# Optimization experiments

Measured on AMD Instinct MI355X. Metric: run time of the kernel, lower is better.

Reference implementation:

```python
import jax, jax.numpy as jnp
import numpy as np

SELF_DIM = 64
OBST_DIM = 32
NUM_LANDMARKS = 8
HID = 128
IN_DIM = SELF_DIM + OBST_DIM  # 96


def setup_inputs() -> dict:
    key = jax.random.key(0)
    ks = jax.random.split(key, 16)
    B = 1024
    obs = jax.random.normal(ks[0], (B, 1, SELF_DIM + 40 + NUM_LANDMARKS * OBST_DIM), dtype=jnp.float32)

    def w(k, shape, fan_in):
        return (jax.random.normal(k, shape, dtype=jnp.float32) / np.sqrt(fan_in)).astype(jnp.float32)

    return {
        "obs": obs,
        "all_neighbor_obs_size": 40,
        "batch_size": B,
        # Hypernet2: Linear(96->128), tanh, Linear(128->96*128), tanh
        "hw1": w(ks[1], (IN_DIM, HID), IN_DIM), "hb1": jnp.zeros((HID,), jnp.float32),
        "hw2": w(ks[2], (HID, IN_DIM * HID), HID), "hb2": jnp.zeros((IN_DIM * HID,), jnp.float32),
        # neighbor_value_mlp: two Linear(128->128) with tanh
        "vw1": w(ks[3], (HID, HID), HID), "vb1": jnp.zeros((HID,), jnp.float32),
        "vw2": w(ks[4], (HID, HID), HID), "vb2": jnp.zeros((HID,), jnp.float32),
        # attention_mlp: Linear(256->128) tanh, Linear(128->128) tanh, Linear(128->1)
        "aw1": w(ks[5], (2 * HID, HID), 2 * HID), "ab1": jnp.zeros((HID,), jnp.float32),
        "aw2": w(ks[6], (HID, HID), HID), "ab2": jnp.zeros((HID,), jnp.float32),
        "aw3": w(ks[7], (HID, 1), HID), "ab3": jnp.zeros((1,), jnp.float32),
    }


def reference(obs, all_neighbor_obs_size, batch_size,
              hw1, hb1, hw2, hb2, vw1, vb1, vw2, vb2,
              aw1, ab1, aw2, ab2, aw3, ab3):
    B = batch_size
    A = obs.shape[1]  # agents per row (1)
    L = NUM_LANDMARKS

    # slice obstacle block and flatten to per-obstacle rows  [B*A*L, OBST_DIM]
    obs_obstacles = obs[:, :, SELF_DIM + all_neighbor_obs_size:].reshape(-1, OBST_DIM)
    # repeat self-obs along dim 1 (torch .repeat(1, L, 1)) -> [B*A*L, SELF_DIM]
    self_rep = jnp.tile(obs[:, :, :SELF_DIM], (1, L, 1)).reshape(-1, SELF_DIM)
    mlp_input = jnp.concatenate([self_rep, obs_obstacles], axis=1)  # [N, 96]
    N = mlp_input.shape[0]

    # Hypernet2 -> per-instance weight [N, 96, HID]
    h = jnp.tanh(mlp_input @ hw1 + hb1)
    w_flat = jnp.tanh(h @ hw2 + hb2)
    obstacle_w = w_flat.reshape(N, IN_DIM, HID)

    # per-instance matvec + tanh  [N, HID]
    emb = jnp.tanh(jnp.einsum('ni,nio->no', mlp_input, obstacle_w))

    # neighbor value MLP
    vals = jnp.tanh(jnp.tanh(emb @ vw1 + vb1) @ vw2 + vb2)

    # mean pooling over landmarks per batch
    emb_mean = emb.reshape(B, -1, HID).mean(axis=1)  # [B, HID]
    # torch mean.repeat(L, 1): tile whole batch block L times (faithful ordering)
    mean_rep = jnp.tile(emb_mean, (L, 1))  # [B*L, HID]

    att_in = jnp.concatenate([emb, mean_rep], axis=1)  # [N, 2*HID]
    a = jnp.tanh(att_in @ aw1 + ab1)
    a = jnp.tanh(a @ aw2 + ab2)
    logits = (a @ aw3 + ab3).reshape(B, -1)  # [B, L]
    att = jax.nn.softmax(logits, axis=1).reshape(-1, 1)  # [N, 1]

    final = (att * vals).reshape(B, -1, HID).sum(axis=1)  # [B, HID]
    return final.reshape(-1, A, HID)
```

## Files before the change

kernel.cpp:

```cpp
#include <hip/hip_runtime.h>

typedef _Float16 f16x8 __attribute__((ext_vector_type(8)));
typedef float f32x4 __attribute__((ext_vector_type(4)));
typedef const __attribute__((address_space(1))) void* as1_cvp;
typedef __attribute__((address_space(3))) void* as3_vp;

__device__ __forceinline__ float tanh_fast(float x){
  float e = __builtin_amdgcn_exp2f(x * 2.88539008177793f);
  return 1.f - 2.f * __builtin_amdgcn_rcpf(1.f + e);
}
__device__ __forceinline__ unsigned short f2h(float f){
  return __builtin_bit_cast(unsigned short, (_Float16)f);
}
__device__ __forceinline__ float h2f(unsigned short u){
  return (float)__builtin_bit_cast(_Float16, u);
}
__device__ __forceinline__ f32x4 mfma16(f16x8 a, f16x8 b, f32x4 c){
  return __builtin_amdgcn_mfma_f32_16x16x32_f16(a, b, c, 0, 0, 0);
}

__device__ __forceinline__ f16x8 ldsA(const unsigned short* buf, int rb, int s, int lane){
  return *(const f16x8*)(buf + (rb*16 + (lane&15))*128 + s*32 + ((lane>>4)<<3));
}

__global__ __launch_bounds__(256) void prep_kernel(
    const float* __restrict__ obs, const float* __restrict__ hw1,
    const float* __restrict__ hb1, const float* __restrict__ hw2,
    const float* __restrict__ vw1, const float* __restrict__ vw2,
    const float* __restrict__ aw1, const float* __restrict__ aw2,
    unsigned short* __restrict__ wt2, unsigned short* __restrict__ vw1t,
    unsigned short* __restrict__ vw2t, unsigned short* __restrict__ aw1t,
    unsigned short* __restrict__ aw2t, unsigned short* __restrict__ h16){
  int b = blockIdx.x, t = threadIdx.x;
  if (b < 1616){
    __shared__ float tile[32][33];
    const float* in; unsigned short* out; int R, C, bx, by; bool swz;
    if (b < 1536)      { in=hw2; out=wt2;  R=128; C=12288; bx=b%384;      by=b/384; swz=true; }
    else if (b < 1552) { int q=b-1536; in=vw1; out=vw1t; R=128; C=128; bx=q&3; by=q>>2; swz=false; }
    else if (b < 1568) { int q=b-1552; in=vw2; out=vw2t; R=128; C=128; bx=q&3; by=q>>2; swz=false; }
    else if (b < 1600) { int q=b-1568; in=aw1; out=aw1t; R=256; C=128; bx=q&3; by=q>>2; swz=false; }
    else               { int q=b-1600; in=aw2; out=aw2t; R=128; C=128; bx=q&3; by=q>>2; swz=false; }
    int c0=bx*32, r0=by*32, tx=t&31, ty=t>>5;
    #pragma unroll
    for (int j=ty; j<32; j+=8) tile[j][tx] = in[(size_t)(r0+j)*C + c0 + tx];
    __syncthreads();
    if (swz){
      #pragma unroll
      for (int j=ty; j<32; j+=8){
        int col = c0+j, k = r0+tx;
        int ig = col>>7, colL = col&127;
        out[(size_t)ig*16384 + colL*128 + (k ^ ((colL&7)<<3))] = f2h(tile[tx][j]);
      }
    } else {
      #pragma unroll
      for (int j=ty; j<32; j+=8) out[(size_t)(c0+j)*R + r0 + tx] = f2h(tile[tx][j]);
    }
  } else {
    __shared__ float w_s[96*128];
    __shared__ float x_s[32*96];
    __shared__ float b_s[128];
    int n0 = (b-1616)*32;
    for (int idx=t; idx<96*128; idx+=256) w_s[idx] = hw1[idx];
    if (t < 128) b_s[t] = hb1[t];
    for (int idx=t; idx<32*96; idx+=256){
      int r = idx/96, i = idx - r*96;
      int n = n0 + r; int bb = n>>3, l = n&7;
      x_s[idx] = (i<64) ? obs[bb*360 + i] : obs[bb*360 + 104 + (l<<5) + (i-64)];
    }
    __syncthreads();
    for (int e=t; e<32*128; e+=256){
      int r = e>>7, o = e&127;
      float acc = b_s[o];
      const float* xr = &x_s[r*96];
      #pragma unroll 4
      for (int i=0;i<96;++i) acc = fmaf(xr[i], w_s[i*128+o], acc);
      h16[(size_t)(n0+r)*128 + o] = f2h(tanh_fast(acc));
    }
  }
}

__device__ __forceinline__ void stage_tile(const unsigned short* gsrc,
                                           unsigned short* lbuf, int t){
  const unsigned short* g = gsrc + t*8;
  unsigned short* l = lbuf + t*8;
  #pragma unroll
  for (int p=0;p<4;++p)
    __builtin_amdgcn_global_load_lds((as1_cvp)(g + p*4096), (as3_vp)(l + p*4096), 16, 0, 0);
}

__global__ __launch_bounds__(512, 2) void k2_hyper(const float* __restrict__ obs,
    const unsigned short* __restrict__ h16, const unsigned short* __restrict__ wt2,
    const float* __restrict__ hb2, float* __restrict__ accg){
  __shared__ unsigned short bts[2][16384];
  __shared__ float x_s[24*128];
  int t = threadIdx.x, lane = t & 63, w = t >> 6;
  int rt = blockIdx.x >> 2, iq = blockIdx.x & 3;
  int R0 = rt*128, ibase = iq*24;
  int rg = w & 3, cg = w >> 2;
  int cl   = lane & 15;
  int kof  = (lane>>4) << 3;
  int rloc = (lane>>4) << 2;

  for (int idx=t; idx<24*128; idx+=512){
    int il = idx>>7, r = idx&127;
    int i = ibase + il;
    int n = R0 + r; int bb = n>>3, l = n&7;
    x_s[idx] = (i<64) ? obs[bb*360 + i] : obs[bb*360 + 104 + (l<<5) + (i-64)];
  }

  f16x8 af[2][4];
  #pragma unroll
  for (int rb=0; rb<2; ++rb)
    #pragma unroll
    for (int s=0; s<4; ++s)
      af[rb][s] = *(const f16x8*)(h16 + (size_t)(R0 + rg*32 + rb*16 + cl)*128 + s*32 + kof);

  stage_tile(wt2 + (size_t)ibase*16384, bts[0], t);
  __syncthreads();

  float facc[2][4][4];
  #pragma unroll
  for (int rb=0;rb<2;++rb)
    #pragma unroll
    for (int ch=0;ch<4;++ch)
      #pragma unroll
      for (int reg=0;reg<4;++reg) facc[rb][ch][reg] = 0.f;

  for (int it=0; it<24; ++it){
    const unsigned short* lb = bts[it&1];
    if (it < 23) stage_tile(wt2 + (size_t)(ibase+it+1)*16384, bts[(it+1)&1], t);
    const float* bias_p = hb2 + (ibase+it)*128;
    float xa[4], xb[4];
    #pragma unroll
    for (int reg=0;reg<4;++reg){
      xa[reg] = x_s[it*128 + rg*32 + rloc + reg];
      xb[reg] = x_s[it*128 + rg*32 + 16 + rloc + reg];
    }
    #pragma unroll
    for (int ch=0; ch<4; ++ch){
      int colL = cg*64 + ch*16 + cl;
      int sx = (colL&7)<<3;
      const unsigned short* bp = lb + colL*128;
      f16x8 b0 = *(const f16x8*)(bp + ((  0+kof)^sx));
      f16x8 b1 = *(const f16x8*)(bp + (( 32+kof)^sx));
      f16x8 b2 = *(const f16x8*)(bp + (( 64+kof)^sx));
      f16x8 b3 = *(const f16x8*)(bp + (( 96+kof)^sx));
      float bi = bias_p[colL];
      f32x4 a0 = {bi,bi,bi,bi}, a1 = {bi,bi,bi,bi};
      a0 = mfma16(af[0][0], b0, a0); a1 = mfma16(af[1][0], b0, a1);
      a0 = mfma16(af[0][1], b1, a0); a1 = mfma16(af[1][1], b1, a1);
      a0 = mfma16(af[0][2], b2, a0); a1 = mfma16(af[1][2], b2, a1);
      a0 = mfma16(af[0][3], b3, a0); a1 = mfma16(af[1][3], b3, a1);
      #pragma unroll
      for (int reg=0;reg<4;++reg){
        facc[0][ch][reg] = fmaf(xa[reg], tanh_fast(a0[reg]), facc[0][ch][reg]);
        facc[1][ch][reg] = fmaf(xb[reg], tanh_fast(a1[reg]), facc[1][ch][reg]);
      }
    }
    __syncthreads();
  }

  #pragma unroll
  for (int rb=0; rb<2; ++rb)
    #pragma unroll
    for (int ch=0; ch<4; ++ch)
      #pragma unroll
      for (int reg=0; reg<4; ++reg)
        atomicAdd(&accg[(size_t)(R0 + rg*32 + rb*16 + rloc + reg)*128 + cg*64 + ch*16 + cl],
                  facc[rb][ch][reg]);
}

__global__ __launch_bounds__(256) void k3_mean(const float* __restrict__ accg,
    unsigned short* __restrict__ mean16){
  int t = threadIdx.x, B0 = blockIdx.x*4;
  for (int task=t; task<512; task+=256){
    int bl = task>>7, o = task&127;
    float m = 0.f;
    #pragma unroll
    for (int l=0;l<8;++l)
      m += tanh_fast(accg[(size_t)((B0 + bl)*8 + l)*128 + o]);
    mean16[(size_t)(B0 + bl)*128 + o] = f2h(m * 0.125f);
  }
}

template<int KS>
__device__ __forceinline__ void stage(const unsigned short* inA, const unsigned short* inB,
    const unsigned short* wt, const float* bias, unsigned short* outb, int w, int lane){
  #pragma unroll
  for (int obl=0; obl<2; ++obl){
    int col = ((w*2+obl)<<4) + (lane&15);
    f32x4 a0 = {0.f,0.f,0.f,0.f}, a1v = {0.f,0.f,0.f,0.f};
    #pragma unroll
    for (int s=0;s<KS;++s){
      f16x8 bfr = *(const f16x8*)(wt + (size_t)col*(KS*32) + s*32 + ((lane>>4)<<3));
      f16x8 aa0, aa1;
      if (KS==8 && s>=4){ aa0 = ldsA(inB,0,s-4,lane); aa1 = ldsA(inB,1,s-4,lane); }
      else              { aa0 = ldsA(inA,0,s,lane);   aa1 = ldsA(inA,1,s,lane);   }
      a0  = mfma16(aa0, bfr, a0);
      a1v = mfma16(aa1, bfr, a1v);
    }
    float bb = bias[col];
    #pragma unroll
    for (int reg=0;reg<4;++reg){
      int r0 = ((lane>>4)<<2) + reg;
      outb[r0*128 + col]      = f2h(tanh_fast(a0[reg] + bb));
      outb[(16+r0)*128 + col] = f2h(tanh_fast(a1v[reg] + bb));
    }
  }
}

__global__ __launch_bounds__(256) void k4_mlp(
    const float* __restrict__ accg, const unsigned short* __restrict__ mean16,
    const unsigned short* __restrict__ vw1t, const unsigned short* __restrict__ vw2t,
    const unsigned short* __restrict__ aw1t, const unsigned short* __restrict__ aw2t,
    const float* __restrict__ vb1, const float* __restrict__ vb2,
    const float* __restrict__ ab1, const float* __restrict__ ab2,
    const float* __restrict__ aw3, const float* __restrict__ ab3,
    float* __restrict__ outp){
  __shared__ unsigned short bufE[32*128];
  __shared__ unsigned short bufM[32*128];
  __shared__ unsigned short bufA[32*128];
  __shared__ float fin[4*128];
  __shared__ float lp[32*8];
  __shared__ float att_s[32];
  int t = threadIdx.x, lane = t&63, w = t>>6;
  int R0 = blockIdx.x*32;

  for (int idx=t; idx<4096; idx+=256)
    bufE[idx] = f2h(tanh_fast(accg[(size_t)R0*128 + idx]));
  for (int idx=t; idx<512; idx+=256){
    int r = idx>>4, c8 = (idx&15)<<3;
    int n = R0 + r;
    *(uint4*)(bufM + r*128 + c8) = *(const uint4*)(mean16 + (size_t)(n & 1023)*128 + c8);
  }
  for (int idx=t; idx<512; idx+=256) fin[idx] = 0.f;
  __syncthreads();

  stage<8>(bufE, bufM, aw1t, ab1, bufA, w, lane);
  __syncthreads();
  stage<4>(bufA, nullptr, aw2t, ab2, bufM, w, lane);
  __syncthreads();
  {
    int r = t>>3, seg = t&7;
    float p = 0.f;
    const unsigned short* row = bufM + r*128 + seg*16;
    const float* w3 = aw3 + seg*16;
    #pragma unroll
    for (int k=0;k<16;++k) p += h2f(row[k]) * w3[k];
    lp[r*8+seg] = p;
  }
  __syncthreads();
  if (t < 4){
    float lg[8]; float mx = -1e30f;
    for (int l=0;l<8;++l){
      float s = ab3[0];
      #pragma unroll
      for (int sg=0;sg<8;++sg) s += lp[(t*8+l)*8+sg];
      lg[l] = s; mx = fmaxf(mx, s);
    }
    float sum = 0.f;
    for (int l=0;l<8;++l){ lg[l] = __builtin_amdgcn_exp2f((lg[l]-mx)*1.44269504089f); sum += lg[l]; }
    float inv = __builtin_amdgcn_rcpf(sum);
    for (int l=0;l<8;++l) att_s[t*8+l] = lg[l]*inv;
  }
  __syncthreads();
  stage<4>(bufE, nullptr, vw1t, vb1, bufA, w, lane);
  __syncthreads();
  {
    #pragma unroll
    for (int obl=0; obl<2; ++obl){
      int col = ((w*2+obl)<<4) + (lane&15);
      f32x4 a0 = {0.f,0.f,0.f,0.f}, a1v = {0.f,0.f,0.f,0.f};
      #pragma unroll
      for (int s=0;s<4;++s){
        f16x8 bfr = *(const f16x8*)(vw2t + (size_t)col*128 + s*32 + ((lane>>4)<<3));
        a0  = mfma16(ldsA(bufA,0,s,lane), bfr, a0);
        a1v = mfma16(ldsA(bufA,1,s,lane), bfr, a1v);
      }
      float bb = vb2[col];
      #pragma unroll
      for (int reg=0;reg<4;++reg){
        int r0 = ((lane>>4)<<2) + reg;
        float v0 = tanh_fast(a0[reg]+bb);
        float v1 = tanh_fast(a1v[reg]+bb);
        atomicAdd(&fin[((r0)>>3)*128 + col],    att_s[r0]    * v0);
        atomicAdd(&fin[((16+r0)>>3)*128 + col], att_s[16+r0] * v1);
      }
    }
  }
  __syncthreads();
  for (int idx=t; idx<512; idx+=256){
    int b_loc = idx>>7, o = idx&127;
    outp[(size_t)(R0/8 + b_loc)*128 + o] = fin[idx];
  }
}

extern "C" void kernel_launch(void* const* d_in, const int* in_sizes, int n_in,
                              void* d_out, int out_size, void* d_ws, size_t ws_size,
                              hipStream_t stream){
  const float* obs = (const float*)d_in[0];
  const float* hw1 = (const float*)d_in[3];
  const float* hb1 = (const float*)d_in[4];
  const float* hw2 = (const float*)d_in[5];
  const float* hb2 = (const float*)d_in[6];
  const float* vw1 = (const float*)d_in[7];
  const float* vb1 = (const float*)d_in[8];
  const float* vw2 = (const float*)d_in[9];
  const float* vb2 = (const float*)d_in[10];
  const float* aw1 = (const float*)d_in[11];
  const float* ab1 = (const float*)d_in[12];
  const float* aw2 = (const float*)d_in[13];
  const float* ab2 = (const float*)d_in[14];
  const float* aw3 = (const float*)d_in[15];
  const float* ab3 = (const float*)d_in[16];

  char* ws = (char*)d_ws;
  unsigned short* wt2    = (unsigned short*)(ws);
  unsigned short* mean16 = (unsigned short*)(ws);
  unsigned short* h16    = (unsigned short*)(ws + 3145728);
  float*          accg   = (float*)        (ws + 5242880);
  unsigned short* vw1t   = (unsigned short*)(ws + 9437184);
  unsigned short* vw2t   = (unsigned short*)(ws + 9469952);
  unsigned short* aw1t   = (unsigned short*)(ws + 9502720);
  unsigned short* aw2t   = (unsigned short*)(ws + 9568256);
  float* outp = (float*)d_out;

  hipMemsetAsync(accg, 0, 8192*128*sizeof(float), stream);
  prep_kernel<<<1872, 256, 0, stream>>>(obs, hw1, hb1, hw2, vw1, vw2, aw1, aw2,
                                        wt2, vw1t, vw2t, aw1t, aw2t, h16);
  k2_hyper<<<256, 512, 0, stream>>>(obs, h16, wt2, hb2, accg);
  k3_mean<<<256, 256, 0, stream>>>(accg, mean16);
  k4_mlp<<<256, 256, 0, stream>>>(accg, mean16, vw1t, vw2t, aw1t, aw2t,
                                  vb1, vb2, ab1, ab2, aw3, ab3, outp);
}
```

Baseline: 121.2 us.

## Split hypernet kernel into smaller blocks over column halves with transposed x

Re-partitions k2_hyper from 256 blocks of 512 threads into 1024 blocks of 256 threads. Each block now covers one 64-column half and 12 input features instead of 24. The weight layout in prep is changed to match the column-half tiles with a new XOR swizzle. Prep also writes a transposed copy of the input features, so k2 loads x as vectors from global memory instead of staging it in LDS. The aim is more parallelism and occupancy with lower LDS use, at the cost of twice as many atomic adds into accg, reloading the h16 A fragments in more blocks, and an extra xT buffer.

Result: slower. 124.5 us (+2.7%).

```diff
diff --git a/kernel.cpp b/kernel.cpp
--- a/kernel.cpp
+++ b/kernel.cpp
@@ -30,7 +30,8 @@
     const float* __restrict__ aw1, const float* __restrict__ aw2,
     unsigned short* __restrict__ wt2, unsigned short* __restrict__ vw1t,
     unsigned short* __restrict__ vw2t, unsigned short* __restrict__ aw1t,
-    unsigned short* __restrict__ aw2t, unsigned short* __restrict__ h16){
+    unsigned short* __restrict__ aw2t, unsigned short* __restrict__ h16,
+    float* __restrict__ xT){
   int b = blockIdx.x, t = threadIdx.x;
   if (b < 1616){
     __shared__ float tile[32][33];
@@ -48,8 +49,9 @@
       #pragma unroll
       for (int j=ty; j<32; j+=8){
         int col = c0+j, k = r0+tx;
-        int ig = col>>7, colL = col&127;
-        out[(size_t)ig*16384 + colL*128 + (k ^ ((colL&7)<<3))] = f2h(tile[tx][j]);
+        int i = col>>7, colL = col&127;
+        int chalf = colL>>6, c64 = colL&63;
+        out[(size_t)(i*2 + chalf)*8192 + c64*128 + (k ^ ((col&15)<<3))] = f2h(tile[tx][j]);
       }
     } else {
       #pragma unroll
@@ -57,7 +59,7 @@
     }
   } else {
     __shared__ float w_s[96*128];
-    __shared__ float x_s[32*96];
+    __shared__ float x_s[32*97];
     __shared__ float b_s[128];
     int n0 = (b-1616)*32;
     for (int idx=t; idx<96*128; idx+=256) w_s[idx] = hw1[idx];
@@ -65,13 +67,17 @@
     for (int idx=t; idx<32*96; idx+=256){
       int r = idx/96, i = idx - r*96;
       int n = n0 + r; int bb = n>>3, l = n&7;
-      x_s[idx] = (i<64) ? obs[bb*360 + i] : obs[bb*360 + 104 + (l<<5) + (i-64)];
+      x_s[r*97+i] = (i<64) ? obs[bb*360 + i] : obs[bb*360 + 104 + (l<<5) + (i-64)];
     }
     __syncthreads();
+    for (int e=t; e<96*32; e+=256){
+      int i = e>>5, r = e&31;
+      xT[(size_t)i*8192 + n0 + r] = x_s[r*97 + i];
+    }
     for (int e=t; e<32*128; e+=256){
       int r = e>>7, o = e&127;
       float acc = b_s[o];
-      const float* xr = &x_s[r*96];
+      const float* xr = &x_s[r*97];
       #pragma unroll 4
       for (int i=0;i<96;++i) acc = fmaf(xr[i], w_s[i*128+o], acc);
       h16[(size_t)(n0+r)*128 + o] = f2h(tanh_fast(acc));
@@ -85,28 +91,22 @@
   unsigned short* l = lbuf + t*8;
   #pragma unroll
   for (int p=0;p<4;++p)
-    __builtin_amdgcn_global_load_lds((as1_cvp)(g + p*4096), (as3_vp)(l + p*4096), 16, 0, 0);
-}
-
-__global__ __launch_bounds__(512, 2) void k2_hyper(const float* __restrict__ obs,
-    const unsigned short* __restrict__ h16, const unsigned short* __restrict__ wt2,
-    const float* __restrict__ hb2, float* __restrict__ accg){
-  __shared__ unsigned short bts[2][16384];
-  __shared__ float x_s[24*128];
-  int t = threadIdx.x, lane = t & 63, w = t >> 6;
-  int rt = blockIdx.x >> 2, iq = blockIdx.x & 3;
-  int R0 = rt*128, ibase = iq*24;
-  int rg = w & 3, cg = w >> 2;
+    __builtin_amdgcn_global_load_lds((as1_cvp)(g + p*2048), (as3_vp)(l + p*2048), 16, 0, 0);
+}
+
+__global__ __launch_bounds__(256, 4) void k2_hyper(
+    const float* __restrict__ xT, const unsigned short* __restrict__ h16,
+    const unsigned short* __restrict__ wt2, const float* __restrict__ hb2,
+    float* __restrict__ accg){
+  __shared__ unsigned short bts[2][8192];
+  int t = threadIdx.x, lane = t & 63, rg = t >> 6;
+  int bid = blockIdx.x;
+  int rt = bid >> 4, chalf = (bid >> 3) & 1, iseg = bid & 7;
+  int R0 = rt*128, C0 = chalf*64, ibase = iseg*12;
   int cl   = lane & 15;
   int kof  = (lane>>4) << 3;
   int rloc = (lane>>4) << 2;
-
-  for (int idx=t; idx<24*128; idx+=512){
-    int il = idx>>7, r = idx&127;
-    int i = ibase + il;
-    int n = R0 + r; int bb = n>>3, l = n&7;
-    x_s[idx] = (i<64) ? obs[bb*360 + i] : obs[bb*360 + 104 + (l<<5) + (i-64)];
-  }
+  int sx   = cl << 3;
 
   f16x8 af[2][4];
   #pragma unroll
@@ -115,7 +115,7 @@
     for (int s=0; s<4; ++s)
       af[rb][s] = *(const f16x8*)(h16 + (size_t)(R0 + rg*32 + rb*16 + cl)*128 + s*32 + kof);
 
-  stage_tile(wt2 + (size_t)ibase*16384, bts[0], t);
+  stage_tile(wt2 + (size_t)(ibase*2 + chalf)*8192, bts[0], t);
   __syncthreads();
 
   float facc[2][4][4];
@@ -126,26 +126,21 @@
       #pragma unroll
       for (int reg=0;reg<4;++reg) facc[rb][ch][reg] = 0.f;
 
-  for (int it=0; it<24; ++it){
+  for (int it=0; it<12; ++it){
     const unsigned short* lb = bts[it&1];
-    if (it < 23) stage_tile(wt2 + (size_t)(ibase+it+1)*16384, bts[(it+1)&1], t);
-    const float* bias_p = hb2 + (ibase+it)*128;
-    float xa[4], xb[4];
-    #pragma unroll
-    for (int reg=0;reg<4;++reg){
-      xa[reg] = x_s[it*128 + rg*32 + rloc + reg];
-      xb[reg] = x_s[it*128 + rg*32 + 16 + rloc + reg];
-    }
+    if (it < 11) stage_tile(wt2 + (size_t)((ibase+it+1)*2 + chalf)*8192, bts[(it+1)&1], t);
+    f32x4 xa = *(const f32x4*)(xT + (size_t)(ibase+it)*8192 + R0 + rg*32 + rloc);
+    f32x4 xb = *(const f32x4*)(xT + (size_t)(ibase+it)*8192 + R0 + rg*32 + 16 + rloc);
+    const float* bias_p = hb2 + (ibase+it)*128 + C0;
     #pragma unroll
     for (int ch=0; ch<4; ++ch){
-      int colL = cg*64 + ch*16 + cl;
-      int sx = (colL&7)<<3;
-      const unsigned short* bp = lb + colL*128;
+      int c64 = ch*16 + cl;
+      const unsigned short* bp = lb + c64*128;
       f16x8 b0 = *(const f16x8*)(bp + ((  0+kof)^sx));
       f16x8 b1 = *(const f16x8*)(bp + (( 32+kof)^sx));
       f16x8 b2 = *(const f16x8*)(bp + (( 64+kof)^sx));
       f16x8 b3 = *(const f16x8*)(bp + (( 96+kof)^sx));
-      float bi = bias_p[colL];
+      float bi = bias_p[c64];
       f32x4 a0 = {bi,bi,bi,bi}, a1 = {bi,bi,bi,bi};
       a0 = mfma16(af[0][0], b0, a0); a1 = mfma16(af[1][0], b0, a1);
       a0 = mfma16(af[0][1], b1, a0); a1 = mfma16(af[1][1], b1, a1);
@@ -166,7 +161,7 @@
     for (int ch=0; ch<4; ++ch)
       #pragma unroll
       for (int reg=0; reg<4; ++reg)
-        atomicAdd(&accg[(size_t)(R0 + rg*32 + rb*16 + rloc + reg)*128 + cg*64 + ch*16 + cl],
+        atomicAdd(&accg[(size_t)(R0 + rg*32 + rb*16 + rloc + reg)*128 + C0 + ch*16 + cl],
                   facc[rb][ch][reg]);
 }
 
@@ -319,16 +314,17 @@
   unsigned short* mean16 = (unsigned short*)(ws);
   unsigned short* h16    = (unsigned short*)(ws + 3145728);
   float*          accg   = (float*)        (ws + 5242880);
-  unsigned short* vw1t   = (unsigned short*)(ws + 9437184);
-  unsigned short* vw2t   = (unsigned short*)(ws + 9469952);
-  unsigned short* aw1t   = (unsigned short*)(ws + 9502720);
-  unsigned short* aw2t   = (unsigned short*)(ws + 9568256);
+  float*          xT     = (float*)        (ws + 9437184);
+  unsigned short* vw1t   = (unsigned short*)(ws + 12582912);
+  unsigned short* vw2t   = (unsigned short*)(ws + 12615680);
+  unsigned short* aw1t   = (unsigned short*)(ws + 12648448);
+  unsigned short* aw2t   = (unsigned short*)(ws + 12713984);
   float* outp = (float*)d_out;
 
   hipMemsetAsync(accg, 0, 8192*128*sizeof(float), stream);
   prep_kernel<<<1872, 256, 0, stream>>>(obs, hw1, hb1, hw2, vw1, vw2, aw1, aw2,
-                                        wt2, vw1t, vw2t, aw1t, aw2t, h16);
-  k2_hyper<<<256, 512, 0, stream>>>(obs, h16, wt2, hb2, accg);
+                                        wt2, vw1t, vw2t, aw1t, aw2t, h16, xT);
+  k2_hyper<<<1024, 256, 0, stream>>>(xT, h16, wt2, hb2, accg);
   k3_mean<<<256, 256, 0, stream>>>(accg, mean16);
   k4_mlp<<<256, 256, 0, stream>>>(accg, mean16, vw1t, vw2t, aw1t, aw2t,
                                   vb1, vb2, ab1, ab2, aw3, ab3, outp);
```
